# Kernel tuning notes

Measured on AMD Instinct MI355X. Metric: run time of the kernel, lower is better.

## Reference

```python
import jax, jax.numpy as jnp
import numpy as np

B, T, DIM, H, DH = 4, 2048, 1024, 16, 64
NEG = -1.0e9


def setup_inputs() -> dict:
    key = jax.random.key(0)
    ks = jax.random.split(key, 12)
    inner = H * DH
    s_in = 1.0 / np.sqrt(DIM)
    s_out = 1.0 / np.sqrt(inner)
    q = jax.random.normal(ks[0], (B, T, DIM), jnp.float32)
    k = jax.random.normal(ks[1], (B, T, DIM), jnp.float32)
    v = jax.random.normal(ks[2], (B, T, DIM), jnp.float32)
    # nn.Linear weights stored as [out, in]; we keep [in, out] for x @ W
    W_q = jax.random.uniform(ks[3], (DIM, inner), jnp.float32, -s_in, s_in)
    b_q = jax.random.uniform(ks[4], (inner,), jnp.float32, -s_in, s_in)
    W_k = jax.random.uniform(ks[5], (DIM, inner), jnp.float32, -s_in, s_in)
    b_k = jax.random.uniform(ks[6], (inner,), jnp.float32, -s_in, s_in)
    W_v = jax.random.uniform(ks[7], (DIM, inner), jnp.float32, -s_in, s_in)
    b_v = jax.random.uniform(ks[8], (inner,), jnp.float32, -s_in, s_in)
    W_o = jax.random.uniform(ks[9], (inner, DIM), jnp.float32, -s_out, s_out)
    b_o = jax.random.uniform(ks[10], (DIM,), jnp.float32, -s_out, s_out)
    # causal mask: True = masked (strict upper triangle), broadcastable [1,1,T,T]
    causal_mask = jnp.triu(jnp.ones((T, T), bool), k=1)[None, None]
    # context mask: True = keep; random padding pattern with col 0 always valid
    context_mask = jax.random.bernoulli(ks[11], 0.9, (B, T)).at[:, 0].set(True)
    return {"q": q, "k": k, "v": v,
            "W_q": W_q, "b_q": b_q, "W_k": W_k, "b_k": b_k,
            "W_v": W_v, "b_v": b_v, "W_o": W_o, "b_o": b_o,
            "causal_mask": causal_mask, "context_mask": context_mask}


def reference(q, k, v, W_q, b_q, W_k, b_k, W_v, b_v, W_o, b_o,
              causal_mask, context_mask):
    scale = DH ** -0.5
    split = lambda x: x.reshape(x.shape[0], x.shape[1], H, DH).transpose(0, 2, 1, 3)
    qh = split(q @ W_q + b_q)  # [b,h,t,d]
    kh = split(k @ W_k + b_k)
    vh = split(v @ W_v + b_v)
    scores = jnp.einsum('bhid,bhjd->bhij', qh * scale, kh)
    scores = jnp.where(context_mask[:, None, None, :], scores, NEG)
    scores = jnp.where(causal_mask, NEG, scores)
    probs = jax.nn.softmax(scores, axis=-1)
    out = jnp.einsum('bhij,bhjd->bhid', probs, vh)
    out = out.transpose(0, 2, 1, 3).reshape(B, T, H * DH)
    return out @ W_o + b_o
```

## Files before the change

### kernel.cpp

```cpp
#include <hip/hip_runtime.h>
#include <hip/hip_bf16.h>
#include <cstdint>
#include <cstddef>

#define DEV static __device__ __forceinline__

typedef __attribute__((ext_vector_type(8))) short short8;
typedef __attribute__((ext_vector_type(4))) short short4v;
typedef __attribute__((ext_vector_type(4))) float floatx4;

#define BB 4
#define TT 2048
#define DIMM 1024
#define HH 16
#define DHH 64
#define MM (BB*TT)
#define QBLK 128
#define NQT (TT/QBLK)
#define M0F 12.0f

DEV unsigned short f2bu(float f) {
    unsigned int u = __float_as_uint(f);
    unsigned int r = (u + 0x7fffu + ((u >> 16) & 1u)) >> 16;
    return (unsigned short)r;
}

DEV unsigned long long pack4(float a, float b, float c, float d) {
    return (unsigned long long)f2bu(a) | ((unsigned long long)f2bu(b) << 16) |
           ((unsigned long long)f2bu(c) << 32) | ((unsigned long long)f2bu(d) << 48);
}

DEV unsigned int pk2(float lo, float hi) {
    __hip_bfloat162 h = __float22bfloat162_rn(make_float2(lo, hi));
    unsigned int r;
    __builtin_memcpy(&r, &h, 4);
    return r;
}

DEV unsigned long long pk4(float a, float b, float c, float d) {
    return (unsigned long long)pk2(a, b) | ((unsigned long long)pk2(c, d) << 32);
}

#if defined(__has_builtin)
#if __has_builtin(__builtin_amdgcn_exp2f)
#define EXP2R(x) __builtin_amdgcn_exp2f(x)
#endif
#endif
#ifndef EXP2R
#define EXP2R(x) exp2f(x)
#endif

DEV void gload16(const void* g, void* l) {
    __builtin_amdgcn_global_load_lds(
        (const __attribute__((address_space(1))) unsigned int*)g,
        (__attribute__((address_space(3))) unsigned int*)l, 16, 0, 0);
}

#define MFMA16(a, b, c) __builtin_amdgcn_mfma_f32_16x16x32_bf16((a), (b), (c), 0, 0, 0)

#if defined(__has_builtin)
#if __has_builtin(__builtin_amdgcn_mfma_f32_16x16x16bf16_1k)
#define HAVE_MFMA_K16 1
#endif
#endif

DEV floatx4 mfma_k16(short4v a, short4v b, floatx4 c) {
#ifdef HAVE_MFMA_K16
    return __builtin_amdgcn_mfma_f32_16x16x16bf16_1k(a, b, c, 0, 0, 0);
#else
    asm volatile("v_mfma_f32_16x16x16_bf16 %0, %1, %2, %0" : "+v"(c) : "v"(a), "v"(b));
    return c;
#endif
}

__global__ __launch_bounds__(256) void ctx_bias(const unsigned char* __restrict__ raw,
                                                float* __restrict__ out) {
    __shared__ int nz1, nz23;
    if (threadIdx.x == 0) { nz1 = 0; nz23 = 0; }
    __syncthreads();
    int a1 = 0, a23 = 0;
    for (int i = threadIdx.x; i < BB * TT; i += 256) {
        unsigned char vb = raw[i];
        int m = i & 3;
        if (vb) { if (m == 1) a1 = 1; else if (m >= 2) a23 = 1; }
    }
    if (a1) atomicOr(&nz1, 1);
    if (a23) atomicOr(&nz23, 1);
    __syncthreads();
    const int mode = nz1 ? 2 : (nz23 ? 1 : 0);
    for (int i = threadIdx.x; i < BB * TT; i += 256) {
        bool keep;
        if (mode == 2)      keep = raw[i] != 0;
        else if (mode == 0) keep = raw[(size_t)4 * i] != 0;
        else                keep = (raw[(size_t)4 * i + 2] | raw[(size_t)4 * i + 3]) != 0;
        out[i] = keep ? -M0F : -3.0e38f;
    }
}

__global__ __launch_bounds__(256) void wtrans(const float* __restrict__ W0, const float* __restrict__ W1,
                                              const float* __restrict__ W2, const float* __restrict__ W3,
                                              unsigned short* __restrict__ out) {
    const float* W = blockIdx.y == 0 ? W0 : blockIdx.y == 1 ? W1 : blockIdx.y == 2 ? W2 : W3;
    unsigned short* O = out + (size_t)blockIdx.y * DIMM * DIMM;
    const int tx = blockIdx.x & 15, ty = blockIdx.x >> 4;
    __shared__ float s[64][65];
    const int tid = threadIdx.x;
#pragma unroll
    for (int j = 0; j < 4; ++j) {
        int c = tid + 256 * j;
        int r = c >> 4, c4 = c & 15;
        float4 vv = *reinterpret_cast<const float4*>(&W[(size_t)(ty * 64 + r) * DIMM + tx * 64 + c4 * 4]);
        s[r][c4 * 4 + 0] = vv.x; s[r][c4 * 4 + 1] = vv.y;
        s[r][c4 * 4 + 2] = vv.z; s[r][c4 * 4 + 3] = vv.w;
    }
    __syncthreads();
#pragma unroll
    for (int j = 0; j < 4; ++j) {
        int c = tid + 256 * j;
        int n = c >> 4, k4 = c & 15;
        unsigned long long pk = pack4(s[k4 * 4 + 0][n], s[k4 * 4 + 1][n], s[k4 * 4 + 2][n], s[k4 * 4 + 3][n]);
        *reinterpret_cast<unsigned long long*>(&O[(size_t)(tx * 64 + n) * DIMM + ty * 64 + k4 * 4]) = pk;
    }
}

__global__ __launch_bounds__(256) void cvt3(const float* __restrict__ q, const float* __restrict__ k,
                                            const float* __restrict__ v,
                                            unsigned short* __restrict__ oq, unsigned short* __restrict__ ok,
                                            unsigned short* __restrict__ ov) {
    const int z = blockIdx.y;
    const float* in = z == 0 ? q : z == 1 ? k : v;
    unsigned short* out = z == 0 ? oq : z == 1 ? ok : ov;
    const size_t i = ((size_t)blockIdx.x * 256 + threadIdx.x) * 8;
    float4 a = *reinterpret_cast<const float4*>(&in[i]);
    float4 b = *reinterpret_cast<const float4*>(&in[i + 4]);
    unsigned long long lo = pk4(a.x, a.y, a.z, a.w);
    unsigned long long hi = pk4(b.x, b.y, b.z, b.w);
    ulonglong2 w; w.x = lo; w.y = hi;
    *reinterpret_cast<ulonglong2*>(&out[i]) = w;
}

__global__ __launch_bounds__(256) void proj3(const unsigned short* __restrict__ Aq,
                                             const unsigned short* __restrict__ Ak,
                                             const unsigned short* __restrict__ Av,
                                             const unsigned short* __restrict__ Wt,
                                             const float* __restrict__ bq, const float* __restrict__ bk,
                                             const float* __restrict__ bv,
                                             unsigned short* __restrict__ Qp, unsigned short* __restrict__ Kp,
                                             unsigned short* __restrict__ Vtp, float scale_q) {
    const int z = blockIdx.z;
    const unsigned short* Ab = z == 0 ? Aq : z == 1 ? Ak : Av;
    const unsigned short* Bt = Wt + (size_t)z * DIMM * DIMM;
    const float* bias = z == 0 ? bq : z == 1 ? bk : bv;
    const float scale = z == 0 ? scale_q : 1.f;

    __shared__ unsigned short As[2][128 * 64];
    __shared__ unsigned short Bs[2][128 * 64];
    const int tid = threadIdx.x, lane = tid & 63, g = lane >> 4, lq = lane & 15;
    const int wid = tid >> 6;
    const int mbase = blockIdx.x * 128, nbase = blockIdx.y * 128;
    const int wm = (wid >> 1) * 64, wn = (wid & 1) * 64;
    floatx4 acc[4][4];
#pragma unroll
    for (int i = 0; i < 4; ++i)
#pragma unroll
        for (int j = 0; j < 4; ++j) acc[i][j] = (floatx4){0.f, 0.f, 0.f, 0.f};

#define STAGE(buf, k0)                                                              \
    {                                                                               \
        _Pragma("unroll")                                                           \
        for (int j = 0; j < 4; ++j) {                                               \
            const int c = j * 256 + tid;                                            \
            const int row = c >> 3, ci = c & 7;                                     \
            const int sc = ci ^ (row & 7);                                          \
            gload16(&Ab[(size_t)(mbase + row) * DIMM + (k0) + sc * 8], &As[buf][c * 8]); \
            gload16(&Bt[(size_t)(nbase + row) * DIMM + (k0) + sc * 8], &Bs[buf][c * 8]); \
        }                                                                           \
    }

    STAGE(0, 0);
    asm volatile("s_waitcnt vmcnt(0)");
    __syncthreads();
    int cur = 0;
    for (int k0 = 0; k0 < DIMM; k0 += 64) {
        if (k0 + 64 < DIMM) STAGE(cur ^ 1, k0 + 64);
#pragma unroll
        for (int kk = 0; kk < 2; ++kk) {
            short8 af[4], bf[4];
#pragma unroll
            for (int i = 0; i < 4; ++i) {
                const int ra = wm + i * 16 + lq;
                af[i] = *reinterpret_cast<const short8*>(&As[cur][ra * 64 + ((kk * 4 + g) ^ (ra & 7)) * 8]);
                const int rb = wn + i * 16 + lq;
                bf[i] = *reinterpret_cast<const short8*>(&Bs[cur][rb * 64 + ((kk * 4 + g) ^ (rb & 7)) * 8]);
            }
#pragma unroll
            for (int i = 0; i < 4; ++i)
#pragma unroll
                for (int j2 = 0; j2 < 4; ++j2)
                    acc[i][j2] = MFMA16(af[i], bf[j2], acc[i][j2]);
        }
        __syncthreads();
        cur ^= 1;
    }
#undef STAGE

#pragma unroll
    for (int i = 0; i < 4; ++i) {
#pragma unroll
        for (int j = 0; j < 4; ++j) {
            const int col = nbase + wn + j * 16 + lq;
            const float bvv = bias[col];
            const int row0 = mbase + wm + i * 16 + g * 4;
            if (z < 2) {
                unsigned short* C = z == 0 ? Qp : Kp;
#pragma unroll
                for (int r = 0; r < 4; ++r)
                    C[(size_t)(row0 + r) * DIMM + col] = f2bu((acc[i][j][r] + bvv) * scale);
            } else {
                const int b = row0 >> 11, t0 = row0 & (TT - 1);
                const int h = col >> 6, d = col & 63;
                unsigned long long pk = pk4(acc[i][j][0] + bvv, acc[i][j][1] + bvv,
                                            acc[i][j][2] + bvv, acc[i][j][3] + bvv);
                *reinterpret_cast<unsigned long long*>(
                    &Vtp[((size_t)(b * HH + h) * DHH + d) * TT + t0]) = pk;
            }
        }
    }
}

__global__ __launch_bounds__(256) void gemm_out(const unsigned short* __restrict__ Ab,
                                                const unsigned short* __restrict__ Bt,
                                                const float* __restrict__ bias,
                                                float* __restrict__ C) {
    __shared__ unsigned short As[2][128 * 64];
    __shared__ unsigned short Bs[2][128 * 64];
    const int tid = threadIdx.x, lane = tid & 63, g = lane >> 4, lq = lane & 15;
    const int wid = tid >> 6;
    const int mbase = blockIdx.x * 128, nbase = blockIdx.y * 128;
    const int wm = (wid >> 1) * 64, wn = (wid & 1) * 64;
    floatx4 acc[4][4];
#pragma unroll
    for (int i = 0; i < 4; ++i)
#pragma unroll
        for (int j = 0; j < 4; ++j) acc[i][j] = (floatx4){0.f, 0.f, 0.f, 0.f};

#define STAGE(buf, k0)                                                              \
    {                                                                               \
        _Pragma("unroll")                                                           \
        for (int j = 0; j < 4; ++j) {                                               \
            const int c = j * 256 + tid;                                            \
            const int row = c >> 3, ci = c & 7;                                     \
            const int sc = ci ^ (row & 7);                                          \
            gload16(&Ab[(size_t)(mbase + row) * DIMM + (k0) + sc * 8], &As[buf][c * 8]); \
            gload16(&Bt[(size_t)(nbase + row) * DIMM + (k0) + sc * 8], &Bs[buf][c * 8]); \
        }                                                                           \
    }

    STAGE(0, 0);
    asm volatile("s_waitcnt vmcnt(0)");
    __syncthreads();
    int cur = 0;
    for (int k0 = 0; k0 < DIMM; k0 += 64) {
        if (k0 + 64 < DIMM) STAGE(cur ^ 1, k0 + 64);
#pragma unroll
        for (int kk = 0; kk < 2; ++kk) {
            short8 af[4], bf[4];
#pragma unroll
            for (int i = 0; i < 4; ++i) {
                const int ra = wm + i * 16 + lq;
                af[i] = *reinterpret_cast<const short8*>(&As[cur][ra * 64 + ((kk * 4 + g) ^ (ra & 7)) * 8]);
                const int rb = wn + i * 16 + lq;
                bf[i] = *reinterpret_cast<const short8*>(&Bs[cur][rb * 64 + ((kk * 4 + g) ^ (rb & 7)) * 8]);
            }
#pragma unroll
            for (int i = 0; i < 4; ++i)
#pragma unroll
                for (int j2 = 0; j2 < 4; ++j2)
                    acc[i][j2] = MFMA16(af[i], bf[j2], acc[i][j2]);
        }
        __syncthreads();
        cur ^= 1;
    }
#undef STAGE

#pragma unroll
    for (int i = 0; i < 4; ++i) {
#pragma unroll
        for (int j = 0; j < 4; ++j) {
            const int col = nbase + wn + j * 16 + lq;
            const float bv = bias[col];
            const int row0 = mbase + wm + i * 16 + g * 4;
#pragma unroll
            for (int r = 0; r < 4; ++r)
                C[(size_t)(row0 + r) * DIMM + col] = acc[i][j][r] + bv;
        }
    }
}

__global__ __launch_bounds__(512, 4) void attn128(const unsigned short* __restrict__ Q,
                                                  const unsigned short* __restrict__ Km,
                                                  const unsigned short* __restrict__ Vt,
                                                  const float* __restrict__ ctxb,
                                                  unsigned short* __restrict__ O) {
    const int pair = blockIdx.x >> 6, h = blockIdx.x & 15, b = (blockIdx.x >> 4) & 3;
    const int tid = threadIdx.x, lane = tid & 63, g = lane >> 4, lq = lane & 15, wid = tid >> 6;

    __shared__ unsigned short Qs[QBLK * 64];
    __shared__ unsigned short Ks[2][64 * 64];
    __shared__ unsigned short Vs[2][64 * 64];
    __shared__ float sbias[TT];

    const unsigned short* Vbase = Vt + (size_t)(b * HH + h) * DHH * TT;
    const int srow = tid >> 3, sdc = tid & 7;
    const int soff = (srow * 128 + sdc * 16) ^ ((srow & 7) << 4);
    const short4v vone = {(short)0x3F80, (short)0x3F80, (short)0x3F80, (short)0x3F80};

    *reinterpret_cast<float4*>(&sbias[tid * 4]) =
        *reinterpret_cast<const float4*>(&ctxb[b * TT + tid * 4]);

    for (int part = 0; part < 2; ++part) {
        const int qt = (part == 0) ? pair : (NQT - 1 - pair);
        const int qbase = qt * QBLK;
        const size_t rowQ = (size_t)(b * TT + qbase);
        const int nkv = 2 * qt + 2;

        __syncthreads();
#pragma unroll
        for (int j = 0; j < 2; ++j) {
            int ci = j * 512 + tid;
            int row = ci >> 3, dc = ci & 7;
            *reinterpret_cast<float4*>((char*)Qs + ((row * 128 + dc * 16) ^ ((row & 7) << 4))) =
                *reinterpret_cast<const float4*>(&Q[(rowQ + row) * DIMM + h * DHH + dc * 8]);
        }
        {
            float4 k0v = *reinterpret_cast<const float4*>(&Km[(size_t)(b * TT + srow) * DIMM + h * DHH + sdc * 8]);
            float4 v0v = *reinterpret_cast<const float4*>(&Vbase[(size_t)srow * TT + sdc * 8]);
            *reinterpret_cast<float4*>((char*)Ks[0] + soff) = k0v;
            *reinterpret_cast<float4*>((char*)Vs[0] + soff) = v0v;
        }
        __syncthreads();

        short8 qf0, qf1;
        {
            const int r = wid * 16 + lq;
            const int sw = (r & 7) << 4;
            qf0 = *reinterpret_cast<const short8*>((char*)Qs + ((r * 128 + g * 16) ^ sw));
            qf1 = *reinterpret_cast<const short8*>((char*)Qs + ((r * 128 + 64 + g * 16) ^ sw));
        }

        floatx4 oacc[4];
#pragma unroll
        for (int f = 0; f < 4; ++f) oacc[f] = (floatx4){0.f, 0.f, 0.f, 0.f};
        floatx4 lacc = (floatx4){0.f, 0.f, 0.f, 0.f};
        const int qwave_min = qbase + wid * 16;
        const int qg = qwave_min + lq;

        for (int kt = 0; kt < nkv; ++kt) {
            const int cur = kt & 1;
            const int kvb = kt * 64;
            const bool pf = (kt + 1 < nkv);
            float4 kreg, vreg;
            if (pf) {
                const int kvn = kvb + 64;
                kreg = *reinterpret_cast<const float4*>(&Km[(size_t)(b * TT + kvn + srow) * DIMM + h * DHH + sdc * 8]);
                vreg = *reinterpret_cast<const float4*>(&Vbase[(size_t)srow * TT + kvn + sdc * 8]);
            }
            if (kvb <= qwave_min + 15) {
                const bool needC = (kvb + 63 > qwave_min);
                float p[4][4];
                __builtin_amdgcn_s_setprio(1);
#pragma unroll
                for (int f = 0; f < 4; ++f) {
                    const int r = f * 16 + lq;
                    const int sw = (r & 7) << 4;
                    short8 kf0 = *reinterpret_cast<const short8*>((char*)Ks[cur] + ((r * 128 + g * 16) ^ sw));
                    short8 kf1 = *reinterpret_cast<const short8*>((char*)Ks[cur] + ((r * 128 + 64 + g * 16) ^ sw));
                    const float4 bias = *reinterpret_cast<const float4*>(&sbias[kvb + f * 16 + g * 4]);
                    floatx4 t = (floatx4){bias.x, bias.y, bias.z, bias.w};
                    t = MFMA16(kf0, qf0, t);
                    t = MFMA16(kf1, qf1, t);
#pragma unroll
                    for (int r2 = 0; r2 < 4; ++r2) {
                        float sv = t[r2];
                        if (needC) {
                            const int kv = kvb + f * 16 + g * 4 + r2;
                            if (kv > qg) sv = -3.0e38f;
                        }
                        p[f][r2] = EXP2R(sv);
                    }
                }
                __builtin_amdgcn_s_setprio(0);
                short4v w[4];
#pragma unroll
                for (int f = 0; f < 4; ++f) {
                    unsigned long long pw = pk4(p[f][0], p[f][1], p[f][2], p[f][3]);
                    __builtin_memcpy(&w[f], &pw, 8);
                }
                __builtin_amdgcn_s_setprio(1);
#pragma unroll
                for (int f = 0; f < 4; ++f) {
                    const int r = f * 16 + lq;
                    const int sw = (r & 7) << 4;
                    const int rb = r * 128;
#pragma unroll
                    for (int j = 0; j < 4; ++j) {
                        short4v av = *reinterpret_cast<const short4v*>(
                            (char*)Vs[cur] + ((rb + j * 32 + g * 8) ^ sw));
                        oacc[f] = mfma_k16(av, w[j], oacc[f]);
                    }
                }
#pragma unroll
                for (int j = 0; j < 4; ++j) lacc = mfma_k16(vone, w[j], lacc);
                __builtin_amdgcn_s_setprio(0);
#ifndef HAVE_MFMA_K16
                asm volatile("s_nop 7\ns_nop 7");
#endif
            }
            if (pf) {
                *reinterpret_cast<float4*>((char*)Ks[cur ^ 1] + soff) = kreg;
                *reinterpret_cast<float4*>((char*)Vs[cur ^ 1] + soff) = vreg;
            }
            __syncthreads();
        }

        const float inv = 1.f / lacc[0];
#pragma unroll
        for (int f = 0; f < 4; ++f) {
            unsigned long long pk = pk4(oacc[f][0] * inv, oacc[f][1] * inv,
                                        oacc[f][2] * inv, oacc[f][3] * inv);
            *reinterpret_cast<unsigned long long*>(
                &O[(rowQ + wid * 16 + lq) * DIMM + h * DHH + f * 16 + g * 4]) = pk;
        }
    }
}

extern "C" void kernel_launch(void* const* d_in, const int* in_sizes, int n_in,
                              void* d_out, int out_size, void* d_ws, size_t ws_size,
                              hipStream_t stream) {
    const float* q  = (const float*)d_in[0];
    const float* k  = (const float*)d_in[1];
    const float* v  = (const float*)d_in[2];
    const float* Wq = (const float*)d_in[3];
    const float* bq = (const float*)d_in[4];
    const float* Wk = (const float*)d_in[5];
    const float* bk = (const float*)d_in[6];
    const float* Wv = (const float*)d_in[7];
    const float* bv = (const float*)d_in[8];
    const float* Wo = (const float*)d_in[9];
    const float* bo = (const float*)d_in[10];
    const unsigned char* cmask = (const unsigned char*)d_in[12];

    unsigned short* Qp  = (unsigned short*)d_ws;
    unsigned short* Kp  = Qp + (size_t)MM * DIMM;
    unsigned short* Vtp = Kp + (size_t)MM * DIMM;
    unsigned short* AO  = Vtp + (size_t)MM * DIMM;
    unsigned short* Wt  = AO + (size_t)MM * DIMM;
    float* ctxb = (float*)(Wt + (size_t)4 * DIMM * DIMM);

    unsigned short* dlo = (unsigned short*)d_out;
    unsigned short* dhi = dlo + (size_t)MM * DIMM;

    ctx_bias<<<dim3(1), dim3(256), 0, stream>>>(cmask, ctxb);
    wtrans<<<dim3(256, 4), dim3(256), 0, stream>>>(Wq, Wk, Wv, Wo, Wt);

    const float scale_q = 0.125f * 1.4426950408889634f;

    cvt3<<<dim3(4096, 3), dim3(256), 0, stream>>>(q, k, v, AO, dlo, dhi);
    proj3<<<dim3(64, 8, 3), dim3(256), 0, stream>>>(AO, dlo, dhi, Wt, bq, bk, bv, Qp, Kp, Vtp, scale_q);

    attn128<<<dim3(BB * HH * 8), dim3(512), 0, stream>>>(Qp, Kp, Vtp, ctxb, AO);

    gemm_out<<<dim3(64, 8), dim3(256), 0, stream>>>(AO, Wt + (size_t)3 * DIMM * DIMM, bo, (float*)d_out);
}
```

Before: 199.7 us.

## Rewrite QKV projection GEMM with 256x256 tiles and ping-pong scheduled pipeline

The QKV projection kernel moves from 128x128 tiles with 4 waves to 256x256 tiles with 8 waves. Each wave now computes a 128x64 sub-tile. The K-loop is restructured into half-tile staged loads interleaved with MFMA phases, using explicit barriers, s_setprio, and vmcnt waits so that global loads overlap compute, in the style of HipKittens' 8-wave ping-pong schedule. The goal is higher arithmetic intensity per LDS byte and better latency hiding. The cost is 128KB of LDS, more accumulator registers, and a smaller grid of 384 blocks, which may underfill the CUs.

```diff
diff --git a/kernel.cpp b/kernel.cpp
--- a/kernel.cpp
+++ b/kernel.cpp
@@ -139,7 +139,7 @@
     *reinterpret_cast<ulonglong2*>(&out[i]) = w;
 }
 
-__global__ __launch_bounds__(256) void proj3(const unsigned short* __restrict__ Aq,
+__global__ __launch_bounds__(512) void proj3(const unsigned short* __restrict__ Aq,
                                              const unsigned short* __restrict__ Ak,
                                              const unsigned short* __restrict__ Av,
                                              const unsigned short* __restrict__ Wt,
@@ -153,76 +153,144 @@
     const float* bias = z == 0 ? bq : z == 1 ? bk : bv;
     const float scale = z == 0 ? scale_q : 1.f;
 
-    __shared__ unsigned short As[2][128 * 64];
-    __shared__ unsigned short Bs[2][128 * 64];
+    __shared__ unsigned short Ah[2][2][128 * 64];
+    __shared__ unsigned short Bh[2][2][128 * 64];
+
     const int tid = threadIdx.x, lane = tid & 63, g = lane >> 4, lq = lane & 15;
     const int wid = tid >> 6;
-    const int mbase = blockIdx.x * 128, nbase = blockIdx.y * 128;
-    const int wm = (wid >> 1) * 64, wn = (wid & 1) * 64;
-    floatx4 acc[4][4];
-#pragma unroll
-    for (int i = 0; i < 4; ++i)
+    const int mbase = blockIdx.x * 256, nbase = blockIdx.y * 256;
+    const int wm = (wid >> 2) * 128, wn = (wid & 3) * 64;
+    const int ah = wm >> 7;
+    const int bh = wn >> 7;
+    const int bwr0 = wn & 64;
+    const int cx = lq & 7;
+
+    floatx4 acc[8][4];
+#pragma unroll
+    for (int i = 0; i < 8; ++i)
 #pragma unroll
         for (int j = 0; j < 4; ++j) acc[i][j] = (floatx4){0.f, 0.f, 0.f, 0.f};
 
-#define STAGE(buf, k0)                                                              \
-    {                                                                               \
-        _Pragma("unroll")                                                           \
-        for (int j = 0; j < 4; ++j) {                                               \
-            const int c = j * 256 + tid;                                            \
-            const int row = c >> 3, ci = c & 7;                                     \
-            const int sc = ci ^ (row & 7);                                          \
-            gload16(&Ab[(size_t)(mbase + row) * DIMM + (k0) + sc * 8], &As[buf][c * 8]); \
-            gload16(&Bt[(size_t)(nbase + row) * DIMM + (k0) + sc * 8], &Bs[buf][c * 8]); \
-        }                                                                           \
-    }
-
-    STAGE(0, 0);
-    asm volatile("s_waitcnt vmcnt(0)");
-    __syncthreads();
-    int cur = 0;
-    for (int k0 = 0; k0 < DIMM; k0 += 64) {
-        if (k0 + 64 < DIMM) STAGE(cur ^ 1, k0 + 64);
-#pragma unroll
-        for (int kk = 0; kk < 2; ++kk) {
-            short8 af[4], bf[4];
-#pragma unroll
-            for (int i = 0; i < 4; ++i) {
-                const int ra = wm + i * 16 + lq;
-                af[i] = *reinterpret_cast<const short8*>(&As[cur][ra * 64 + ((kk * 4 + g) ^ (ra & 7)) * 8]);
-                const int rb = wn + i * 16 + lq;
-                bf[i] = *reinterpret_cast<const short8*>(&Bs[cur][rb * 64 + ((kk * 4 + g) ^ (rb & 7)) * 8]);
-            }
-#pragma unroll
-            for (int i = 0; i < 4; ++i)
-#pragma unroll
-                for (int j2 = 0; j2 < 4; ++j2)
-                    acc[i][j2] = MFMA16(af[i], bf[j2], acc[i][j2]);
-        }
-        __syncthreads();
-        cur ^= 1;
-    }
-#undef STAGE
-
-#pragma unroll
-    for (int i = 0; i < 4; ++i) {
-#pragma unroll
-        for (int j = 0; j < 4; ++j) {
-            const int col = nbase + wn + j * 16 + lq;
+    auto stageA = [&](int par, int half, int kt) {
+#pragma unroll
+        for (int j = 0; j < 2; ++j) {
+            const int c = j * 512 + tid;
+            const int row = c >> 3, ci = c & 7;
+            const int sc = ci ^ (row & 7);
+            gload16(&Ab[(size_t)(mbase + half * 128 + row) * DIMM + kt * 64 + sc * 8],
+                    &Ah[par][half][c * 8]);
+        }
+    };
+    auto stageB = [&](int par, int half, int kt) {
+#pragma unroll
+        for (int j = 0; j < 2; ++j) {
+            const int c = j * 512 + tid;
+            const int row = c >> 3, ci = c & 7;
+            const int sc = ci ^ (row & 7);
+            gload16(&Bt[(size_t)(nbase + half * 128 + row) * DIMM + kt * 64 + sc * 8],
+                    &Bh[par][half][c * 8]);
+        }
+    };
+    auto rdA = [&](int par, int rb, int kk) -> short8 {
+        const int ar = rb * 16 + lq;
+        return *reinterpret_cast<const short8*>(&Ah[par][ah][ar * 64 + (((kk << 2) + g) ^ cx) * 8]);
+    };
+    auto rdB = [&](int par, int cb, int kk) -> short8 {
+        const int br = bwr0 + cb * 16 + lq;
+        return *reinterpret_cast<const short8*>(&Bh[par][bh][br * 64 + (((kk << 2) + g) ^ cx) * 8]);
+    };
+
+    short8 b[4][2], aq0[2], aq1[2], an0[2], an1[2];
+
+#define QMFMA(qq, A0_, A1_)                                              \
+    {                                                                    \
+        _Pragma("unroll")                                                \
+        for (int cb = 0; cb < 4; ++cb) {                                 \
+            acc[2*(qq)][cb]   = MFMA16(A0_[0], b[cb][0], acc[2*(qq)][cb]);   \
+            acc[2*(qq)][cb]   = MFMA16(A0_[1], b[cb][1], acc[2*(qq)][cb]);   \
+            acc[2*(qq)+1][cb] = MFMA16(A1_[0], b[cb][0], acc[2*(qq)+1][cb]); \
+            acc[2*(qq)+1][cb] = MFMA16(A1_[1], b[cb][1], acc[2*(qq)+1][cb]); \
+        }                                                                \
+    }
+#define PH_MID()                                   \
+    __builtin_amdgcn_s_barrier();                  \
+    asm volatile("s_waitcnt lgkmcnt(0)");          \
+    __builtin_amdgcn_sched_barrier(0);             \
+    __builtin_amdgcn_s_setprio(1);
+#define PH_END()                                   \
+    __builtin_amdgcn_s_setprio(0);                 \
+    __builtin_amdgcn_s_barrier();
+
+    stageA(0, 0, 0); stageA(0, 1, 0); stageB(0, 0, 0); stageB(0, 1, 0);
+    asm volatile("s_waitcnt vmcnt(4)");
+    stageB(1, 0, 1); stageB(1, 1, 1); stageA(1, 0, 1);
+    asm volatile("s_waitcnt vmcnt(6)");
+    __builtin_amdgcn_s_barrier();
+
+    for (int i = 0; i < 8; ++i) {
+        const int t1 = 2 * i + 1, t2 = 2 * i + 2, t3 = 2 * i + 3;
+        const bool more = (i < 7);
+#pragma unroll
+        for (int cb = 0; cb < 4; ++cb) { b[cb][0] = rdB(0, cb, 0); b[cb][1] = rdB(0, cb, 1); }
+        aq0[0] = rdA(0, 0, 0); aq0[1] = rdA(0, 0, 1);
+        aq1[0] = rdA(0, 1, 0); aq1[1] = rdA(0, 1, 1);
+        stageA(1, 1, t1);
+        PH_MID(); QMFMA(0, aq0, aq1); PH_END();
+        aq0[0] = rdA(0, 2, 0); aq0[1] = rdA(0, 2, 1);
+        aq1[0] = rdA(0, 3, 0); aq1[1] = rdA(0, 3, 1);
+        if (more) stageB(0, 0, t2);
+        PH_MID(); QMFMA(1, aq0, aq1); PH_END();
+        aq0[0] = rdA(0, 4, 0); aq0[1] = rdA(0, 4, 1);
+        aq1[0] = rdA(0, 5, 0); aq1[1] = rdA(0, 5, 1);
+        an0[0] = rdA(0, 6, 0); an0[1] = rdA(0, 6, 1);
+        an1[0] = rdA(0, 7, 0); an1[1] = rdA(0, 7, 1);
+        if (more) stageB(0, 1, t2);
+        PH_MID(); QMFMA(2, aq0, aq1); PH_END();
+        if (more) { stageA(0, 0, t2); asm volatile("s_waitcnt vmcnt(6)"); }
+        else      { asm volatile("s_waitcnt vmcnt(0)"); }
+        PH_MID(); QMFMA(3, an0, an1); PH_END();
+#pragma unroll
+        for (int cb = 0; cb < 4; ++cb) { b[cb][0] = rdB(1, cb, 0); b[cb][1] = rdB(1, cb, 1); }
+        aq0[0] = rdA(1, 0, 0); aq0[1] = rdA(1, 0, 1);
+        aq1[0] = rdA(1, 1, 0); aq1[1] = rdA(1, 1, 1);
+        if (more) stageA(0, 1, t2);
+        PH_MID(); QMFMA(0, aq0, aq1); PH_END();
+        aq0[0] = rdA(1, 2, 0); aq0[1] = rdA(1, 2, 1);
+        aq1[0] = rdA(1, 3, 0); aq1[1] = rdA(1, 3, 1);
+        if (more) stageB(1, 0, t3);
+        PH_MID(); QMFMA(1, aq0, aq1); PH_END();
+        aq0[0] = rdA(1, 4, 0); aq0[1] = rdA(1, 4, 1);
+        aq1[0] = rdA(1, 5, 0); aq1[1] = rdA(1, 5, 1);
+        an0[0] = rdA(1, 6, 0); an0[1] = rdA(1, 6, 1);
+        an1[0] = rdA(1, 7, 0); an1[1] = rdA(1, 7, 1);
+        if (more) stageB(1, 1, t3);
+        PH_MID(); QMFMA(2, aq0, aq1); PH_END();
+        if (more) { stageA(1, 0, t3); asm volatile("s_waitcnt vmcnt(6)"); }
+        PH_MID(); QMFMA(3, an0, an1); PH_END();
+    }
+#undef QMFMA
+#undef PH_MID
+#undef PH_END
+
+#pragma unroll
+    for (int rb = 0; rb < 8; ++rb) {
+#pragma unroll
+        for (int cb = 0; cb < 4; ++cb) {
+            const int col = nbase + wn + cb * 16 + lq;
             const float bvv = bias[col];
-            const int row0 = mbase + wm + i * 16 + g * 4;
+            const int row0 = mbase + wm + rb * 16 + g * 4;
             if (z < 2) {
                 unsigned short* C = z == 0 ? Qp : Kp;
 #pragma unroll
                 for (int r = 0; r < 4; ++r)
-                    C[(size_t)(row0 + r) * DIMM + col] = f2bu((acc[i][j][r] + bvv) * scale);
+                    C[(size_t)(row0 + r) * DIMM + col] = f2bu((acc[rb][cb][r] + bvv) * scale);
             } else {
-                const int b = row0 >> 11, t0 = row0 & (TT - 1);
-                const int h = col >> 6, d = col & 63;
-                unsigned long long pk = pk4(acc[i][j][0] + bvv, acc[i][j][1] + bvv,
-                                            acc[i][j][2] + bvv, acc[i][j][3] + bvv);
+                const int bb = row0 >> 11, t0 = row0 & (TT - 1);
+                const int hh = col >> 6, d = col & 63;
+                unsigned long long pk = pk4(acc[rb][cb][0] + bvv, acc[rb][cb][1] + bvv,
+                                            acc[rb][cb][2] + bvv, acc[rb][cb][3] + bvv);
                 *reinterpret_cast<unsigned long long*>(
-                    &Vtp[((size_t)(b * HH + h) * DHH + d) * TT + t0]) = pk;
+                    &Vtp[((size_t)(bb * HH + hh) * DHH + d) * TT + t0]) = pk;
             }
         }
     }
@@ -466,7 +534,7 @@
     const float scale_q = 0.125f * 1.4426950408889634f;
 
     cvt3<<<dim3(4096, 3), dim3(256), 0, stream>>>(q, k, v, AO, dlo, dhi);
-    proj3<<<dim3(64, 8, 3), dim3(256), 0, stream>>>(AO, dlo, dhi, Wt, bq, bk, bv, Qp, Kp, Vtp, scale_q);
+    proj3<<<dim3(32, 4, 3), dim3(512), 0, stream>>>(AO, dlo, dhi, Wt, bq, bk, bv, Qp, Kp, Vtp, scale_q);
 
     attn128<<<dim3(BB * HH * 8), dim3(512), 0, stream>>>(Qp, Kp, Vtp, ctxb, AO);
 
```

New measurement: 221.1 us. 1.11x slower.
